# Performance work log

Hardware: AMD Instinct MI355X
Metric: run time of the kernel (lower is better)

## Reference

```python
import jax, jax.numpy as jnp
import numpy as np

DEPTH = 8  # remaining_depth at the root
N_INTERNAL = 2**DEPTH - 1  # 255, level-order indexed
N_LEAF = 2**DEPTH          # 256
CLAMP_MIN = 1e-5


def setup_inputs() -> dict:
    key = jax.random.key(0)
    k1, k2, k3 = jax.random.split(key, 3)
    B, D_in, D_out = 65536, 1024, 128
    x = jax.random.normal(k1, (B, D_in), dtype=jnp.float32)
    # one independent Linear(D_in,1) per internal node (deepcopy of split_function),
    # packed into a single [D_in, N_INTERNAL] matrix, level-order
    W_split = jax.random.normal(k2, (D_in, N_INTERNAL), dtype=jnp.float32) * (1.0 / np.sqrt(D_in))
    b_split = jnp.zeros((N_INTERNAL,), dtype=jnp.float32)
    # leaf values: uniform(-a, a) with a = sqrt(6/output_dim), per the torch init
    a = (6.0 / D_out) ** 0.5
    leaf_values = jax.random.uniform(k3, (N_LEAF, D_out), minval=-a, maxval=a, dtype=jnp.float32)
    return {"x": x, "W_split": W_split, "b_split": b_split, "leaf_values": leaf_values}


def reference(x, W_split, b_split, leaf_values):
    B = x.shape[0]
    # gate probability of every internal node in one batched GEMM: [B, N_INTERNAL]
    P = jax.nn.sigmoid(x @ W_split + b_split)
    # accumulate soft routing probability to each leaf, level by level
    probs = jnp.ones((B, 1), dtype=x.dtype)
    for d in range(DEPTH):
        p = P[:, 2**d - 1 : 2**(d + 1) - 1]  # gates at level d: [B, 2^d]
        # child order: left = (1-p), right = p (matches recursion ordering)
        probs = jnp.stack([(1.0 - p) * probs, p * probs], axis=-1).reshape(B, 2**(d + 1))
    out = probs @ leaf_values  # [B, D_out]: sum_leaf path_prob * value
    # regularization: sum over internal nodes of -0.5 * 2^-depth * mean_b log(clamp(p(1-p)))
    weights = jnp.concatenate(
        [jnp.full((2**d,), 2.0 ** (-d), dtype=x.dtype) for d in range(DEPTH)]
    )  # [N_INTERNAL]
    reg = jnp.sum(-0.5 * weights * jnp.mean(jnp.log(jnp.maximum(P * (1.0 - P), CLAMP_MIN)), axis=0))
    return out, reg
```

## Files before the change

kernel.cpp:

```cpp
#include <hip/hip_runtime.h>

#define B_TOT   65536
#define DIN     1024
#define NNODES  255
#define NPAD    256
#define DOUT    128
#define BM      64
#define BK      64
#define NKT     (DIN / BK)

typedef __attribute__((ext_vector_type(8))) _Float16      f16x8;
typedef __attribute__((ext_vector_type(4))) float         f32x4;
typedef __attribute__((ext_vector_type(4))) unsigned short u16x4;
typedef __attribute__((ext_vector_type(8))) unsigned short u16x8;
typedef __attribute__((ext_vector_type(4))) unsigned int   u32x4;
typedef unsigned short u16;
typedef unsigned int   u32;

__device__ __forceinline__ u16 f2h(float f) {
  _Float16 h = (_Float16)f;
  return __builtin_bit_cast(u16, h);
}
__device__ __forceinline__ float h2f(u16 b) {
  return (float)__builtin_bit_cast(_Float16, b);
}
__device__ __forceinline__ u32 pk2h(float a, float b) {
  return __builtin_bit_cast(u32, __builtin_amdgcn_cvt_pkrtz(a, b));
}
__device__ __forceinline__ void cp16_g2s(const float* g, float* l) {
  __builtin_amdgcn_global_load_lds(
      (const __attribute__((address_space(1))) unsigned int*)g,
      (__attribute__((address_space(3))) unsigned int*)l, 16, 0, 0);
}

__device__ __forceinline__ int swzP(int row, int col) {
  int g = col >> 3;
  int gs = (g & ~7) | ((g ^ row) & 7);
  return (row << 8) + (gs << 3) + (col & 7);
}

__global__ void prep_w(const float* __restrict__ Wsp, u16* __restrict__ WtG) {
  __shared__ float t[64][65];
  const int tid = threadIdx.x;
  const int wn = blockIdx.x;
  const int kc = blockIdx.y;
  const int bn = wn * 64, bk = kc * 64;
  {
    int n = tid & 63, kr0 = tid >> 6;
    #pragma unroll
    for (int i = 0; i < 16; ++i) {
      int k = kr0 + i * 4;
      int node = bn + n;
      t[k][n] = (node < NNODES) ? Wsp[(size_t)(bk + k) * NNODES + node] : 0.0f;
    }
  }
  __syncthreads();
  #pragma unroll
  for (int half = 0; half < 2; ++half) {
    int f = half * 256 + tid;
    int nt = f >> 7, rem = f & 127;
    int ks = rem >> 6, rem2 = rem & 63;
    int quad = rem2 >> 4, l15 = rem2 & 15;
    int nl = nt * 16 + l15;
    u16x8 v;
    #pragma unroll
    for (int j = 0; j < 8; ++j)
      v[j] = f2h(t[ks * 32 + quad * 8 + j][nl]);
    size_t F = (size_t)((((kc * 4 + wn) * 4 + nt) * 2 + ks) * 64 + (quad * 16 + l15));
    *(u16x8*)&WtG[F * 8] = v;
  }
}

__global__ void prep_leaf(const float* __restrict__ leaf, u16* __restrict__ lT) {
  int t = blockIdx.x * 256 + threadIdx.x;
  int j = t & 127, l = t >> 7;
  lT[j * NPAD + l] = f2h(leaf[l * DOUT + j]);
}

__global__ void finalize(const float* __restrict__ pw, float* __restrict__ regp) {
  int t = threadIdx.x;
  float s = 0.0f;
  #pragma unroll
  for (int i = 0; i < 8; ++i) s += pw[i * 512 + t];
  #pragma unroll
  for (int off = 32; off > 0; off >>= 1) s += __shfl_down(s, off, 64);
  __shared__ float red[8];
  if ((t & 63) == 0) red[t >> 6] = s;
  __syncthreads();
  if (t == 0) {
    float tot = 0.0f;
    #pragma unroll
    for (int i = 0; i < 8; ++i) tot += red[i];
    *regp = tot * (-0.5f / 65536.0f);
  }
}

__global__ __launch_bounds__(256, 4) void fused_sdt(
    const float* __restrict__ x, const float* __restrict__ bsp,
    const u16* __restrict__ WtG, const u16* __restrict__ lT,
    float* __restrict__ out, float* __restrict__ pw)
{
  __shared__ char smem[32768] __attribute__((aligned(16)));
  float* xs0 = (float*)smem;
  float* xs1 = xs0 + 4096;
  u16*   PB  = (u16*)smem;

  const int tid  = threadIdx.x;
  const int lane = tid & 63;
  const int w    = tid >> 6;
  const int l15  = lane & 15;
  const int quad = lane >> 4;
  const int wn   = w;
  const int blk  = blockIdx.x;

  const float* xg = x + (size_t)blk * BM * DIN;

  f32x4 acc[4][4];
  #pragma unroll
  for (int mt = 0; mt < 4; ++mt)
    #pragma unroll
    for (int nt = 0; nt < 4; ++nt) {
      f32x4 z = {0.0f, 0.0f, 0.0f, 0.0f};
      acc[mt][nt] = z;
    }

  auto stage_x = [&](float* buf, int kt) {
    #pragma unroll
    for (int i = 0; i < 4; ++i) {
      int s   = (w * 4 + i) * 64 + lane;
      int row = s >> 4;
      int g   = ((s & 15) ^ row) & 15;
      cp16_g2s(xg + (size_t)row * DIN + kt * BK + g * 4,
               buf + (w * 4 + i) * 256);
    }
  };

  stage_x(xs0, 0);
  __syncthreads();

  float* xcur = xs0;
  float* xnxt = xs1;
  for (int kc = 0; kc < NKT; ++kc) {
    f16x8 Bf[8];
    {
      const u16* wbase = WtG + (size_t)kc * 16384 + (size_t)wn * 4096;
      #pragma unroll
      for (int q = 0; q < 8; ++q)
        Bf[q] = *(const f16x8*)&wbase[(q & 3) * 1024 + (q >> 2) * 512 + lane * 8];
    }
    if (kc + 1 < NKT) stage_x(xnxt, kc + 1);
    __builtin_amdgcn_s_setprio(1);
    #pragma unroll
    for (int ks = 0; ks < 2; ++ks) {
      const int g0 = ks * 8 + quad * 2;
      #pragma unroll
      for (int mt = 0; mt < 4; ++mt) {
        const int row = mt * 16 + l15;
        const float* rb = xcur + row * 64;
        f32x4 lo = *(const f32x4*)(rb + (((g0    ) ^ row) & 15) * 4);
        f32x4 hi = *(const f32x4*)(rb + (((g0 + 1) ^ row) & 15) * 4);
        u32x4 aw;
        aw[0] = pk2h(lo[0], lo[1]);
        aw[1] = pk2h(lo[2], lo[3]);
        aw[2] = pk2h(hi[0], hi[1]);
        aw[3] = pk2h(hi[2], hi[3]);
        f16x8 A = __builtin_bit_cast(f16x8, aw);
        #pragma unroll
        for (int nt = 0; nt < 4; ++nt)
          acc[mt][nt] = __builtin_amdgcn_mfma_f32_16x16x32_f16(
              A, Bf[ks * 4 + nt], acc[mt][nt], 0, 0, 0);
      }
    }
    __builtin_amdgcn_s_setprio(0);
    __syncthreads();
    float* tsw = xcur; xcur = xnxt; xnxt = tsw;
  }

  float rsum = 0.0f;
  float bv[4];
  #pragma unroll
  for (int nt = 0; nt < 4; ++nt) {
    int c = wn * 64 + nt * 16 + l15;
    bv[nt] = (c < NNODES) ? bsp[c] : 0.0f;
  }
  #pragma unroll
  for (int mt = 0; mt < 4; ++mt) {
    #pragma unroll
    for (int nt = 0; nt < 4; ++nt) {
      int c = wn * 64 + nt * 16 + l15;
      #pragma unroll
      for (int r = 0; r < 4; ++r) {
        int row = mt * 16 + quad * 4 + r;
        float z = acc[mt][nt][r] + bv[nt];
        float e = __expf(-z);
        float p = __builtin_amdgcn_rcpf(1.0f + e);
        PB[swzP(row, c)] = f2h(p);
        if (c < NNODES) {
          float v = fmaxf(p * (1.0f - p), 1e-5f);
          int d = 31 - __clz(c + 1);
          float wgt = __builtin_bit_cast(float, (u32)(127 - d) << 23);
          rsum += wgt * __logf(v);
        }
      }
    }
  }
  #pragma unroll
  for (int off = 32; off > 0; off >>= 1) rsum += __shfl_down(rsum, off, 64);
  if (lane == 0) pw[blk * 4 + w] = rsum;
  __syncthreads();

  for (int rr = 0; rr < 16; ++rr) {
    int row = (w << 4) + rr;
    float prod = 1.0f;
    #pragma unroll
    for (int d = 0; d < 6; ++d) {
      int node = (1 << d) - 1 + (lane >> (6 - d));
      float pv = h2f(PB[swzP(row, node)]);
      prod *= ((lane >> (5 - d)) & 1) ? pv : (1.0f - pv);
    }
    float p6  = h2f(PB[swzP(row, 63 + lane)]);
    float p7a = h2f(PB[swzP(row, 127 + 2 * lane)]);
    float p7b = h2f(PB[swzP(row, 128 + 2 * lane)]);
    float a0 = prod * (1.0f - p6), a1 = prod * p6;
    u16x4 o;
    o.x = f2h(a0 * (1.0f - p7a));
    o.y = f2h(a0 * p7a);
    o.z = f2h(a1 * (1.0f - p7b));
    o.w = f2h(a1 * p7b);
    *(u16x4*)&PB[swzP(row, 4 * lane)] = o;
  }
  __syncthreads();

  f32x4 acc2[4][2];
  #pragma unroll
  for (int mt = 0; mt < 4; ++mt)
    #pragma unroll
    for (int nt = 0; nt < 2; ++nt) {
      f32x4 z = {0.0f, 0.0f, 0.0f, 0.0f};
      acc2[mt][nt] = z;
    }
  for (int kc = 0; kc < 4; ++kc) {
    #pragma unroll
    for (int ks = 0; ks < 2; ++ks) {
      const int kk = kc * 64 + ks * 32 + quad * 8;
      f16x8 Af[4], Bf2[2];
      #pragma unroll
      for (int nt = 0; nt < 2; ++nt)
        Bf2[nt] = *(const f16x8*)&lT[(wn * 32 + nt * 16 + l15) * NPAD + kk];
      #pragma unroll
      for (int mt = 0; mt < 4; ++mt)
        Af[mt] = *(const f16x8*)&PB[swzP(mt * 16 + l15, kk)];
      #pragma unroll
      for (int mt = 0; mt < 4; ++mt)
        #pragma unroll
        for (int nt = 0; nt < 2; ++nt)
          acc2[mt][nt] = __builtin_amdgcn_mfma_f32_16x16x32_f16(
              Af[mt], Bf2[nt], acc2[mt][nt], 0, 0, 0);
    }
  }
  #pragma unroll
  for (int mt = 0; mt < 4; ++mt)
    #pragma unroll
    for (int nt = 0; nt < 2; ++nt)
      #pragma unroll
      for (int r = 0; r < 4; ++r) {
        int row = mt * 16 + quad * 4 + r;
        int col = wn * 32 + nt * 16 + l15;
        out[(size_t)(blk * BM + row) * DOUT + col] = acc2[mt][nt][r];
      }
}

extern "C" void kernel_launch(void* const* d_in, const int* in_sizes, int n_in,
                              void* d_out, int out_size, void* d_ws, size_t ws_size,
                              hipStream_t stream) {
  (void)in_sizes; (void)n_in; (void)out_size; (void)ws_size;
  const float* x    = (const float*)d_in[0];
  const float* Wsp  = (const float*)d_in[1];
  const float* bsp  = (const float*)d_in[2];
  const float* leaf = (const float*)d_in[3];
  float* out  = (float*)d_out;
  float* regp = out + (size_t)B_TOT * DOUT;

  u16* WtG = (u16*)d_ws;
  u16* lT  = WtG + NPAD * DIN;
  float* pw = (float*)(lT + NPAD * DOUT);

  prep_w<<<dim3(4, 16), 256, 0, stream>>>(Wsp, WtG);
  prep_leaf<<<(NPAD * DOUT) / 256, 256, 0, stream>>>(leaf, lT);
  fused_sdt<<<B_TOT / BM, 256, 0, stream>>>(x, bsp, WtG, lT, out, pw);
  finalize<<<1, 512, 0, stream>>>(pw, regp);
}
```

Baseline: 415.2 us.

## Load x fragments directly from global memory instead of LDS double-buffering

Removes the LDS double-buffered staging of x tiles via global_load_lds, along with the per-iteration barrier and priority hints. Each wave now reads its A fragments straight from global memory into registers. Because all four waves share the same x rows, each wave loads them separately, so redundant global/L2 traffic rises fourfold and the loads are no longer overlapped with compute. The gain is fewer barriers and less LDS pressure.

```diff
diff --git a/kernel.cpp b/kernel.cpp
--- a/kernel.cpp
+++ b/kernel.cpp
@@ -27,11 +27,6 @@
 __device__ __forceinline__ u32 pk2h(float a, float b) {
   return __builtin_bit_cast(u32, __builtin_amdgcn_cvt_pkrtz(a, b));
 }
-__device__ __forceinline__ void cp16_g2s(const float* g, float* l) {
-  __builtin_amdgcn_global_load_lds(
-      (const __attribute__((address_space(1))) unsigned int*)g,
-      (__attribute__((address_space(3))) unsigned int*)l, 16, 0, 0);
-}
 
 __device__ __forceinline__ int swzP(int row, int col) {
   int g = col >> 3;
@@ -100,10 +95,7 @@
     const u16* __restrict__ WtG, const u16* __restrict__ lT,
     float* __restrict__ out, float* __restrict__ pw)
 {
-  __shared__ char smem[32768] __attribute__((aligned(16)));
-  float* xs0 = (float*)smem;
-  float* xs1 = xs0 + 4096;
-  u16*   PB  = (u16*)smem;
+  __shared__ u16 PB[BM * 256] __attribute__((aligned(16)));
 
   const int tid  = threadIdx.x;
   const int lane = tid & 63;
@@ -114,6 +106,7 @@
   const int blk  = blockIdx.x;
 
   const float* xg = x + (size_t)blk * BM * DIN;
+  const float* xrow = xg + (size_t)l15 * DIN + quad * 8;
 
   f32x4 acc[4][4];
   #pragma unroll
@@ -124,22 +117,7 @@
       acc[mt][nt] = z;
     }
 
-  auto stage_x = [&](float* buf, int kt) {
-    #pragma unroll
-    for (int i = 0; i < 4; ++i) {
-      int s   = (w * 4 + i) * 64 + lane;
-      int row = s >> 4;
-      int g   = ((s & 15) ^ row) & 15;
-      cp16_g2s(xg + (size_t)row * DIN + kt * BK + g * 4,
-               buf + (w * 4 + i) * 256);
-    }
-  };
-
-  stage_x(xs0, 0);
-  __syncthreads();
-
-  float* xcur = xs0;
-  float* xnxt = xs1;
+  #pragma unroll 1
   for (int kc = 0; kc < NKT; ++kc) {
     f16x8 Bf[8];
     {
@@ -148,17 +126,13 @@
       for (int q = 0; q < 8; ++q)
         Bf[q] = *(const f16x8*)&wbase[(q & 3) * 1024 + (q >> 2) * 512 + lane * 8];
     }
-    if (kc + 1 < NKT) stage_x(xnxt, kc + 1);
-    __builtin_amdgcn_s_setprio(1);
     #pragma unroll
     for (int ks = 0; ks < 2; ++ks) {
-      const int g0 = ks * 8 + quad * 2;
       #pragma unroll
       for (int mt = 0; mt < 4; ++mt) {
-        const int row = mt * 16 + l15;
-        const float* rb = xcur + row * 64;
-        f32x4 lo = *(const f32x4*)(rb + (((g0    ) ^ row) & 15) * 4);
-        f32x4 hi = *(const f32x4*)(rb + (((g0 + 1) ^ row) & 15) * 4);
+        const float* p = xrow + (size_t)(mt * 16) * DIN + kc * 64 + ks * 32;
+        f32x4 lo = *(const f32x4*)(p);
+        f32x4 hi = *(const f32x4*)(p + 4);
         u32x4 aw;
         aw[0] = pk2h(lo[0], lo[1]);
         aw[1] = pk2h(lo[2], lo[3]);
@@ -171,9 +145,6 @@
               A, Bf[ks * 4 + nt], acc[mt][nt], 0, 0, 0);
       }
     }
-    __builtin_amdgcn_s_setprio(0);
-    __syncthreads();
-    float* tsw = xcur; xcur = xnxt; xnxt = tsw;
   }
 
   float rsum = 0.0f;
```

Result: slower. 479.0 us (+15.4%).
